# Performance work log

Measured on AMD Instinct MI355X. Metric: run time of the kernel, lower is better.

The kernel has to match this reference:

```python
import jax, jax.numpy as jnp
import numpy as np

B, H, W, C = 8, 64, 64, 512
G = 32  # num_groups
EPS = 1e-5


def group_norm(x, scale, bias):
    b, h, w, c = x.shape
    xg = x.reshape(b, h, w, G, c // G)
    mean = jnp.mean(xg, axis=(1, 2, 4), keepdims=True)
    var = jnp.var(xg, axis=(1, 2, 4), keepdims=True)
    xg = (xg - mean) / jnp.sqrt(var + EPS)
    x = xg.reshape(b, h, w, c)
    return x * scale + bias


def conv1x1(x, w, b):
    # NHWC 1x1 conv == channel matmul
    return jnp.einsum('bhwc,cd->bhwd', x, w) + b


def setup_inputs() -> dict:
    key = jax.random.key(0)
    ks = jax.random.split(key, 10)
    init = lambda k, shape: jax.random.normal(k, shape, dtype=jnp.float32) * (1.0 / np.sqrt(C))
    return {
        'x': jax.random.normal(ks[0], (B, H, W, C), dtype=jnp.float32),
        'gn_scale': jnp.ones((C,), dtype=jnp.float32),
        'gn_bias': jnp.zeros((C,), dtype=jnp.float32),
        'wq': init(ks[1], (C, C)), 'bq': jnp.zeros((C,), jnp.float32),
        'wk': init(ks[2], (C, C)), 'bk': jnp.zeros((C,), jnp.float32),
        'wv': init(ks[3], (C, C)), 'bv': jnp.zeros((C,), jnp.float32),
        'wo': init(ks[4], (C, C)), 'bo': jnp.zeros((C,), jnp.float32),
    }


def reference(x, gn_scale, gn_bias, wq, bq, wk, bk, wv, bv, wo, bo):
    h = group_norm(x, gn_scale, gn_bias)
    q = conv1x1(h, wq, bq)
    k = conv1x1(h, wk, bk)
    v = conv1x1(h, wv, bv)
    b, hh, ww, c = h.shape
    n = hh * ww
    q = q.reshape(b, n, c)
    k = k.reshape(b, n, c)
    v = v.reshape(b, n, c)
    scores = jnp.einsum('bqc,bkc->bqk', q, k) * (c ** -0.5)
    attn = jax.nn.softmax(scores, axis=-1)
    out = jnp.einsum('bqk,bkc->bqc', attn, v).reshape(b, hh, ww, c)
    out = conv1x1(out, wo, bo)
    return out + x
```

## Files before the change

kernel.cpp:

```cpp
#include <hip/hip_runtime.h>

typedef __bf16 bfx8 __attribute__((ext_vector_type(8)));
typedef __bf16 bfx4 __attribute__((ext_vector_type(4)));
typedef float  f32x4 __attribute__((ext_vector_type(4)));

#define MFMA16(a,b,c) __builtin_amdgcn_mfma_f32_16x16x32_bf16((a),(b),(c),0,0,0)

static constexpr int BATCH = 8;
static constexpr int NTOK  = 4096;
static constexpr int CH    = 512;
static constexpr float GN_EPS = 1e-5f;
static constexpr float ATT_SCALE = 0.044194173824159216f;

__device__ __forceinline__ void gload16(const void* g, void* l)
{
    __builtin_amdgcn_global_load_lds(
        (const __attribute__((address_space(1))) unsigned int*)g,
        (__attribute__((address_space(3))) unsigned int*)l, 16, 0, 0);
}

__global__ __launch_bounds__(256)
void prep_weights(const float* __restrict__ wq, const float* __restrict__ wk,
                  const float* __restrict__ wv, const float* __restrict__ wo,
                  const float* __restrict__ bq, const float* __restrict__ bk,
                  const float* __restrict__ bv,
                  __bf16* __restrict__ wqkvT, __bf16* __restrict__ woT,
                  float* __restrict__ bqkv)
{
    __shared__ __bf16 t[32][36];
    const int z  = blockIdx.z;
    const float* src = (z == 0) ? wq : (z == 1) ? wk : (z == 2) ? wv : wo;
    const int c0 = blockIdx.x * 32, n0 = blockIdx.y * 32;
    const int tid = threadIdx.x;
    const int r = tid >> 3, c4 = (tid & 7) * 4;

    f32x4 in = *(const f32x4*)&src[(size_t)(c0 + r) * 512 + n0 + c4];
    bfx4 tv;
#pragma unroll
    for (int i = 0; i < 4; ++i) tv[i] = (__bf16)in[i];
    *(bfx4*)&t[r][c4] = tv;
    __syncthreads();
    bfx4 o;
#pragma unroll
    for (int i = 0; i < 4; ++i) o[i] = t[c4 + i][r];
    if (z < 3)
        *(bfx4*)&wqkvT[((size_t)(z * 512 + n0 + r)) * 512 + c0 + c4] = o;
    else
        *(bfx4*)&woT[((size_t)(n0 + r)) * 512 + c0 + c4] = o;

    if (z < 3 && blockIdx.x == 0 && blockIdx.y == 0) {
        const float* bs = (z == 0) ? bq : (z == 1) ? bk : bv;
        bqkv[z * 512 + tid]       = bs[tid];
        bqkv[z * 512 + tid + 256] = bs[tid + 256];
    }
}

__global__ __launch_bounds__(256)
void gn_stats(const float* __restrict__ x, const float* __restrict__ gs,
              const float* __restrict__ gb,
              float* __restrict__ scA, float* __restrict__ biA)
{
    const int g = blockIdx.x, b = blockIdx.y;
    const int tid = threadIdx.x;
    const int half = tid & 1;
    const size_t base = (size_t)b * NTOK * CH + g * 16 + half * 8;

    float sum = 0.f, sumsq = 0.f;
    for (int i = tid; i < 2 * NTOK; i += 256) {
        const int s = i >> 1;
        f32x4 v0 = *(const f32x4*)&x[base + (size_t)s * CH];
        f32x4 v1 = *(const f32x4*)&x[base + (size_t)s * CH + 4];
#pragma unroll
        for (int j = 0; j < 4; ++j) {
            sum += v0[j] + v1[j];
            sumsq += v0[j] * v0[j] + v1[j] * v1[j];
        }
    }
#pragma unroll
    for (int o = 32; o; o >>= 1) { sum += __shfl_down(sum, o); sumsq += __shfl_down(sumsq, o); }
    __shared__ float red[8];
    __shared__ float stats[2];
    const int w = tid >> 6;
    if ((tid & 63) == 0) { red[w] = sum; red[4 + w] = sumsq; }
    __syncthreads();
    if (tid == 0) {
        float s1 = red[0] + red[1] + red[2] + red[3];
        float s2 = red[4] + red[5] + red[6] + red[7];
        float mean = s1 * (1.f / 65536.f);
        float var  = s2 * (1.f / 65536.f) - mean * mean;
        stats[0] = mean; stats[1] = rsqrtf(var + GN_EPS);
    }
    __syncthreads();
    if (tid < 16) {
        const int ch = g * 16 + tid;
        const float sc = gs[ch] * stats[1];
        scA[b * 512 + ch] = sc;
        biA[b * 512 + ch] = gb[ch] - stats[0] * sc;
    }
}

__global__ __launch_bounds__(256)
void gemm_qkv(const float* __restrict__ x, const float* __restrict__ scA,
              const float* __restrict__ biA, const __bf16* __restrict__ Bt,
              const float* __restrict__ bias,
              __bf16* __restrict__ qk, __bf16* __restrict__ vT)
{
    const int bm = blockIdx.x * 128, bn = blockIdx.y * 128;
    const int tid = threadIdx.x;
    const int w = tid >> 6, lane = tid & 63, quad = lane >> 4, l15 = lane & 15;
    const int wm = (w >> 1) * 64, wn = (w & 1) * 64;
    const int brow = bm >> 12;

    __shared__ __bf16 sAB[2][128][40];

    f32x4 acc[4][4];
#pragma unroll
    for (int i = 0; i < 4; ++i)
#pragma unroll
        for (int j = 0; j < 4; ++j) acc[i][j] = (f32x4){0.f, 0.f, 0.f, 0.f};

    const int sr = tid >> 2, scol = (tid & 3) * 8;
    for (int k0 = 0; k0 < 512; k0 += 32) {
        __syncthreads();
        {
            const float* scp = scA + brow * 512 + k0 + scol;
            const float* bip = biA + brow * 512 + k0 + scol;
            f32x4 s0v = *(const f32x4*)&scp[0], s1v = *(const f32x4*)&scp[4];
            f32x4 b0v = *(const f32x4*)&bip[0], b1v = *(const f32x4*)&bip[4];
            f32x4 xa0 = *(const f32x4*)&x[(size_t)(bm + sr) * 512 + k0 + scol];
            f32x4 xa1 = *(const f32x4*)&x[(size_t)(bm + sr) * 512 + k0 + scol + 4];
            f32x4 xb0 = *(const f32x4*)&x[(size_t)(bm + sr + 64) * 512 + k0 + scol];
            f32x4 xb1 = *(const f32x4*)&x[(size_t)(bm + sr + 64) * 512 + k0 + scol + 4];
            bfx8 ha, hb;
#pragma unroll
            for (int j = 0; j < 4; ++j) {
                ha[j]     = (__bf16)(xa0[j] * s0v[j] + b0v[j]);
                ha[4 + j] = (__bf16)(xa1[j] * s1v[j] + b1v[j]);
                hb[j]     = (__bf16)(xb0[j] * s0v[j] + b0v[j]);
                hb[4 + j] = (__bf16)(xb1[j] * s1v[j] + b1v[j]);
            }
            *(bfx8*)&sAB[0][sr][scol]      = ha;
            *(bfx8*)&sAB[0][sr + 64][scol] = hb;
        }
        *(bfx8*)&sAB[1][sr][scol]      = *(const bfx8*)&Bt[(size_t)(bn + sr) * 512 + k0 + scol];
        *(bfx8*)&sAB[1][sr + 64][scol] = *(const bfx8*)&Bt[(size_t)(bn + sr + 64) * 512 + k0 + scol];
        __syncthreads();
        bfx8 af[4], bfr[4];
#pragma unroll
        for (int mi = 0; mi < 4; ++mi) af[mi]  = *(const bfx8*)&sAB[0][wm + mi * 16 + l15][quad * 8];
#pragma unroll
        for (int ni = 0; ni < 4; ++ni) bfr[ni] = *(const bfx8*)&sAB[1][wn + ni * 16 + l15][quad * 8];
#pragma unroll
        for (int mi = 0; mi < 4; ++mi)
#pragma unroll
            for (int ni = 0; ni < 4; ++ni)
                acc[mi][ni] = MFMA16(af[mi], bfr[ni], acc[mi][ni]);
    }

    if (blockIdx.y < 8) {
#pragma unroll
        for (int ni = 0; ni < 4; ++ni) {
            const int col = bn + wn + ni * 16 + l15;
            const float bv = bias[col];
#pragma unroll
            for (int mi = 0; mi < 4; ++mi)
#pragma unroll
                for (int rr = 0; rr < 4; ++rr) {
                    const int row = bm + wm + mi * 16 + quad * 4 + rr;
                    qk[(size_t)row * 1024 + col] = (__bf16)(acc[mi][ni][rr] + bv);
                }
        }
    } else {
        const int vch0 = bn - 1024;
        const int tokbase = bm & 4095;
        __bf16* tb = &sAB[0][0][0];
        __syncthreads();
#pragma unroll
        for (int chunk = 0; chunk < 2; ++chunk) {
            if ((w & 1) == chunk) {
#pragma unroll
                for (int ni = 0; ni < 4; ++ni) {
                    const int chc = ni * 16 + l15;
                    const float bv = bias[bn + chunk * 64 + chc];
#pragma unroll
                    for (int mi = 0; mi < 4; ++mi)
#pragma unroll
                        for (int rr = 0; rr < 4; ++rr) {
                            const int tok = wm + mi * 16 + quad * 4 + rr;
                            tb[chc * 136 + tok] = (__bf16)(acc[mi][ni][rr] + bv);
                        }
                }
            }
            __syncthreads();
            {
                const int chn = tid >> 2, t0 = (tid & 3) * 32;
                const size_t gb0 =
                    ((size_t)(brow * 512 + vch0 + chunk * 64 + chn)) * 4096 + tokbase;
#pragma unroll
                for (int u = 0; u < 4; ++u)
                    *(bfx8*)&vT[gb0 + t0 + u * 8] = *(const bfx8*)&tb[chn * 136 + t0 + u * 8];
            }
            __syncthreads();
        }
    }
}

__global__ __launch_bounds__(512, 2)
void attn_fused(const __bf16* __restrict__ qk, const __bf16* __restrict__ vT,
                const __bf16* __restrict__ woT, const float* __restrict__ bo,
                const float* __restrict__ x, float* __restrict__ out)
{
    const int bb = blockIdx.y;
    const int q0 = blockIdx.x * 128;
    const int tid = threadIdx.x;
    const int w = tid >> 6, lane = tid & 63, quad = lane >> 4, l15 = lane & 15;

    __shared__ __attribute__((aligned(16))) unsigned char smem[141312];
    __bf16 (*Ks)[32][512]      = (__bf16(*)[32][512])smem;
    __bf16 (*Vs)[32][4][16][8] = (__bf16(*)[32][4][16][8])(smem + 65536);
    __bf16 (*Ph)[40]           = (__bf16(*)[40])(smem + 131072);
    __bf16 (*Obuf)[520]        = (__bf16(*)[520])smem;

    bfx8 qf[16];
    {
        const __bf16* qptr = qk + ((size_t)(bb * NTOK + q0 + w * 16 + l15)) * 1024;
#pragma unroll
        for (int kk = 0; kk < 16; ++kk)
            qf[kk] = *(const bfx8*)&qptr[kk * 32 + quad * 8];
    }

    f32x4 oacc[32];
#pragma unroll
    for (int i = 0; i < 32; ++i) oacc[i] = (f32x4){0.f, 0.f, 0.f, 0.f};
    float mcur = -1e30f, lcur = 0.f;

#pragma unroll
    for (int u = 0; u < 4; ++u) {
        const int r = w * 4 + u;
        gload16(qk + ((size_t)(bb * NTOK + r)) * 1024 + 512 + ((lane ^ (r & 7)) * 8),
                &Ks[0][r][0]);
    }
#pragma unroll
    for (int u = 0; u < 4; ++u) {
        const int g = w * 4 + u;
        gload16(vT + ((size_t)(bb * 512 + g * 16 + (lane & 15))) * 4096 + (lane >> 4) * 8,
                &Vs[0][g][0][0][0]);
    }

    const int NT = NTOK / 32;
    int buf = 0;
    for (int kt = 0; kt < NT; ++kt) {
        __syncthreads();

        if (kt + 1 < NT) {
            const int kv1 = (kt + 1) * 32;
            const int nb = buf ^ 1;
#pragma unroll
            for (int u = 0; u < 4; ++u) {
                const int r = w * 4 + u;
                gload16(qk + ((size_t)(bb * NTOK + kv1 + r)) * 1024 + 512 + ((lane ^ (r & 7)) * 8),
                        &Ks[nb][r][0]);
            }
#pragma unroll
            for (int u = 0; u < 4; ++u) {
                const int g = w * 4 + u;
                gload16(vT + ((size_t)(bb * 512 + g * 16 + (lane & 15))) * 4096 + kv1 + (lane >> 4) * 8,
                        &Vs[nb][g][0][0][0]);
            }
        }

        f32x4 s0 = (f32x4){0.f, 0.f, 0.f, 0.f}, s1 = (f32x4){0.f, 0.f, 0.f, 0.f};
#pragma unroll
        for (int kk = 0; kk < 16; ++kk) {
            const int pc = (((kk * 4 + quad) ^ (l15 & 7)) * 8);
            bfx8 kb0 = *(const bfx8*)&Ks[buf][l15][pc];
            bfx8 kb1 = *(const bfx8*)&Ks[buf][16 + l15][pc];
            s0 = MFMA16(kb0, qf[kk], s0);
            s1 = MFMA16(kb1, qf[kk], s1);
        }

        float mx = -1e30f;
#pragma unroll
        for (int i = 0; i < 4; ++i) {
            s0[i] *= ATT_SCALE; s1[i] *= ATT_SCALE;
            mx = fmaxf(mx, fmaxf(s0[i], s1[i]));
        }
        mx = fmaxf(mx, __shfl_xor(mx, 16));
        mx = fmaxf(mx, __shfl_xor(mx, 32));
        const float mnew = fmaxf(mcur, mx);
        const float al = __expf(mcur - mnew);
        float ps = 0.f;
        bfx4 pl0, pl1;
#pragma unroll
        for (int i = 0; i < 4; ++i) { float p = __expf(s0[i] - mnew); ps += p; pl0[i] = (__bf16)p; }
#pragma unroll
        for (int i = 0; i < 4; ++i) { float p = __expf(s1[i] - mnew); ps += p; pl1[i] = (__bf16)p; }
        ps += __shfl_xor(ps, 16);
        ps += __shfl_xor(ps, 32);
        lcur = lcur * al + ps;
        mcur = mnew;

        *(bfx4*)&Ph[w * 16 + l15][quad * 4]      = pl0;
        *(bfx4*)&Ph[w * 16 + l15][16 + quad * 4] = pl1;

        if (__any(al != 1.0f)) {
#pragma unroll
            for (int ct = 0; ct < 32; ++ct)
#pragma unroll
                for (int r = 0; r < 4; ++r) oacc[ct][r] *= al;
        }

        asm volatile("s_waitcnt lgkmcnt(0)" ::: "memory");
        bfx8 pa = *(const bfx8*)&Ph[w * 16 + l15][quad * 8];

#pragma unroll
        for (int ct = 0; ct < 32; ++ct) {
            bfx8 vb = *(const bfx8*)&Vs[buf][ct][quad][l15][0];
            oacc[ct] = MFMA16(vb, pa, oacc[ct]);
        }
        buf ^= 1;
    }

#pragma unroll
    for (int h = 0; h < 2; ++h) {
        __syncthreads();
        if ((w >> 2) == h) {
            const float linv = 1.f / lcur;
#pragma unroll
            for (int ct = 0; ct < 32; ++ct) {
                bfx4 ov;
#pragma unroll
                for (int r = 0; r < 4; ++r) ov[r] = (__bf16)(oacc[ct][r] * linv);
                *(bfx4*)&Obuf[(w & 3) * 16 + l15][ct * 16 + quad * 4] = ov;
            }
        }
        __syncthreads();

        const int rs  = (w & 3) * 16;
        const int nt0 = (w >> 2) * 16;
        bfx8 af2[16];
#pragma unroll
        for (int k0 = 0; k0 < 16; ++k0)
            af2[k0] = *(const bfx8*)&Obuf[rs + l15][k0 * 32 + quad * 8];
#pragma unroll 4
        for (int nt = 0; nt < 16; ++nt) {
            f32x4 a2 = (f32x4){0.f, 0.f, 0.f, 0.f};
#pragma unroll
            for (int k0 = 0; k0 < 16; ++k0) {
                bfx8 wb = *(const bfx8*)&woT[(size_t)((nt0 + nt) * 16 + l15) * 512 + k0 * 32 + quad * 8];
                a2 = MFMA16(af2[k0], wb, a2);
            }
            const int col = (nt0 + nt) * 16 + l15;
            const float bv = bo[col];
#pragma unroll
            for (int rr = 0; rr < 4; ++rr) {
                const size_t idx =
                    ((size_t)(bb * NTOK + q0 + h * 64 + rs + quad * 4 + rr)) * 512 + col;
                out[idx] = a2[rr] + bv + x[idx];
            }
        }
    }
}

extern "C" void kernel_launch(void* const* d_in, const int* in_sizes, int n_in,
                              void* d_out, int out_size, void* d_ws, size_t ws_size,
                              hipStream_t stream)
{
    const float* x  = (const float*)d_in[0];
    const float* gs = (const float*)d_in[1];
    const float* gb = (const float*)d_in[2];
    const float* wq = (const float*)d_in[3];
    const float* bq = (const float*)d_in[4];
    const float* wk = (const float*)d_in[5];
    const float* bk = (const float*)d_in[6];
    const float* wv = (const float*)d_in[7];
    const float* bv = (const float*)d_in[8];
    const float* wo = (const float*)d_in[9];
    const float* bo = (const float*)d_in[10];
    float* out = (float*)d_out;

    char* ws = (char*)d_ws;
    __bf16* qk    = (__bf16*)(ws);
    __bf16* vT    = (__bf16*)(ws + 67108864);
    __bf16* wqkvT = (__bf16*)(ws + 100663296);
    __bf16* woT   = (__bf16*)(ws + 102236160);
    float*  bqkv  = (float* )(ws + 102760448);
    float*  scA   = (float* )(ws + 102766592);
    float*  biA   = (float* )(ws + 102782976);

    prep_weights<<<dim3(16, 16, 4), 256, 0, stream>>>(wq, wk, wv, wo, bq, bk, bv,
                                                      wqkvT, woT, bqkv);
    gn_stats<<<dim3(32, BATCH), 256, 0, stream>>>(x, gs, gb, scA, biA);
    gemm_qkv<<<dim3(256, 12), 256, 0, stream>>>(x, scA, biA, wqkvT, bqkv, qk, vT);
    attn_fused<<<dim3(NTOK / 128, BATCH), 512, 0, stream>>>(qk, vT, woT, bo, x, out);
}
```

Baseline: 776.1 us.

## Repartition PV accumulation so each wave owns channel slices across all query rows

The P·V stage is re-tiled. Previously each wave accumulated all 512 output channels for its own 16 query rows. Now each wave owns 64 channels across all 128 query rows, reading the shared P tile for every row block and only its own four V slices. Rescale factors and row sums go through shared memory, with a per-iteration flag and a block barrier, so each wave can apply other waves' softmax corrections. This cuts redundant LDS reads of V per wave, at the cost of an extra workgroup barrier per key tile and more P reads from LDS.

```diff
diff --git a/kernel.cpp b/kernel.cpp
--- a/kernel.cpp
+++ b/kernel.cpp
@@ -215,11 +215,14 @@
     const int tid = threadIdx.x;
     const int w = tid >> 6, lane = tid & 63, quad = lane >> 4, l15 = lane & 15;
 
-    __shared__ __attribute__((aligned(16))) unsigned char smem[141312];
+    __shared__ __attribute__((aligned(16))) unsigned char smem[142352];
     __bf16 (*Ks)[32][512]      = (__bf16(*)[32][512])smem;
     __bf16 (*Vs)[32][4][16][8] = (__bf16(*)[32][4][16][8])(smem + 65536);
     __bf16 (*Ph)[40]           = (__bf16(*)[40])(smem + 131072);
-    __bf16 (*Obuf)[520]        = (__bf16(*)[520])smem;
+    float* abuf  = (float*)(smem + 141312);
+    float* lbuf  = (float*)(smem + 141824);
+    int*   rflag = (int*)(smem + 142336);
+    __bf16 (*Obuf)[520] = (__bf16(*)[520])smem;
 
     bfx8 qf[16];
     {
@@ -229,9 +232,11 @@
             qf[kk] = *(const bfx8*)&qptr[kk * 32 + quad * 8];
     }
 
-    f32x4 oacc[32];
-#pragma unroll
-    for (int i = 0; i < 32; ++i) oacc[i] = (f32x4){0.f, 0.f, 0.f, 0.f};
+    f32x4 oacc[4][8];
+#pragma unroll
+    for (int i = 0; i < 4; ++i)
+#pragma unroll
+        for (int j = 0; j < 8; ++j) oacc[i][j] = (f32x4){0.f, 0.f, 0.f, 0.f};
     float mcur = -1e30f, lcur = 0.f;
 
 #pragma unroll
@@ -302,36 +307,52 @@
 
         *(bfx4*)&Ph[w * 16 + l15][quad * 4]      = pl0;
         *(bfx4*)&Ph[w * 16 + l15][16 + quad * 4] = pl1;
-
-        if (__any(al != 1.0f)) {
-#pragma unroll
-            for (int ct = 0; ct < 32; ++ct)
-#pragma unroll
-                for (int r = 0; r < 4; ++r) oacc[ct][r] *= al;
-        }
-
-        asm volatile("s_waitcnt lgkmcnt(0)" ::: "memory");
-        bfx8 pa = *(const bfx8*)&Ph[w * 16 + l15][quad * 8];
-
-#pragma unroll
-        for (int ct = 0; ct < 32; ++ct) {
-            bfx8 vb = *(const bfx8*)&Vs[buf][ct][quad][l15][0];
-            oacc[ct] = MFMA16(vb, pa, oacc[ct]);
+        if (quad == 0) abuf[w * 16 + l15] = al;
+        if (__ballot(al != 1.0f)) { if (lane == 0) rflag[kt & 1] = 1; }
+        if (tid == 0) rflag[(kt + 1) & 1] = 0;
+
+        asm volatile("s_waitcnt lgkmcnt(0)\n\ts_barrier" ::: "memory");
+
+        if (rflag[kt & 1]) {
+#pragma unroll
+            for (int qt = 0; qt < 8; ++qt) {
+                const float a = abuf[qt * 16 + l15];
+#pragma unroll
+                for (int ct = 0; ct < 4; ++ct)
+#pragma unroll
+                    for (int r = 0; r < 4; ++r) oacc[ct][qt][r] *= a;
+            }
+        }
+
+        bfx8 vb[4];
+#pragma unroll
+        for (int ct = 0; ct < 4; ++ct)
+            vb[ct] = *(const bfx8*)&Vs[buf][w * 4 + ct][quad][l15][0];
+#pragma unroll
+        for (int qt = 0; qt < 8; ++qt) {
+            bfx8 pa = *(const bfx8*)&Ph[qt * 16 + l15][quad * 8];
+#pragma unroll
+            for (int ct = 0; ct < 4; ++ct)
+                oacc[ct][qt] = MFMA16(vb[ct], pa, oacc[ct][qt]);
         }
         buf ^= 1;
     }
 
+    if (quad == 0) lbuf[w * 16 + l15] = lcur;
+
 #pragma unroll
     for (int h = 0; h < 2; ++h) {
         __syncthreads();
-        if ((w >> 2) == h) {
-            const float linv = 1.f / lcur;
-#pragma unroll
-            for (int ct = 0; ct < 32; ++ct) {
+#pragma unroll
+        for (int t = 0; t < 4; ++t) {
+            const int qt = h * 4 + t;
+            const float linv = 1.f / lbuf[qt * 16 + l15];
+#pragma unroll
+            for (int ct = 0; ct < 4; ++ct) {
                 bfx4 ov;
 #pragma unroll
-                for (int r = 0; r < 4; ++r) ov[r] = (__bf16)(oacc[ct][r] * linv);
-                *(bfx4*)&Obuf[(w & 3) * 16 + l15][ct * 16 + quad * 4] = ov;
+                for (int r = 0; r < 4; ++r) ov[r] = (__bf16)(oacc[ct][qt][r] * linv);
+                *(bfx4*)&Obuf[t * 16 + l15][w * 64 + ct * 16 + quad * 4] = ov;
             }
         }
         __syncthreads();
```

Measured after the change: 852.2 us. +9.8%, slower.
